# Kernel optimization log

Measured on AMD Instinct MI355X. Metric: run time of the kernel, lower is better.

Reference implementation:

```python
import jax, jax.numpy as jnp
import numpy as np

N = 50000   # nodes
E = 800000  # edges
F = 16      # raw feature width (sliced 4:10 -> 6)
H = 256     # hidden_dim
O = 128     # out_dim
NE = 4      # n_experts
G = 64      # graphs in batch
K = 2       # top_k
XS, XE = 4, 10
SPS = 0.3   # size_prior_strength


def setup_inputs() -> dict:
    key = jax.random.key(0)
    ks = jax.random.split(key, 16)
    rn = lambda k, s: jax.random.normal(k, s, dtype=jnp.float32) * 0.05
    return dict(
        x=jax.random.normal(ks[0], (N, F), dtype=jnp.float32),
        edge_index=jax.random.randint(ks[1], (2, E), 0, N),
        batch=jnp.sort(jax.random.randint(ks[2], (N,), 0, G)),
        enc_W1=rn(ks[3], (6, H)), enc_b1=jnp.zeros(H, jnp.float32),
        enc_W2=rn(ks[4], (H, H)), enc_b2=jnp.zeros(H, jnp.float32),
        r_W1=rn(ks[5], (H + 3, H)), r_b1=jnp.zeros(H, jnp.float32),
        ln_g=jnp.ones(H, jnp.float32), ln_b=jnp.zeros(H, jnp.float32),
        r_W2=rn(ks[6], (H, NE)), r_b2=jnp.zeros(NE, jnp.float32),
        size_centers=jnp.linspace(0.0, 1.0, NE, dtype=jnp.float32),
        W0_rel=rn(ks[7], (NE, H, H)), b0_rel=jnp.zeros((NE, H), jnp.float32), W0_root=rn(ks[8], (NE, H, H)),
        W1_rel=rn(ks[9], (NE, H, H)), b1_rel=jnp.zeros((NE, H), jnp.float32), W1_root=rn(ks[10], (NE, H, H)),
        W2_rel=rn(ks[11], (NE, H, O)), b2_rel=jnp.zeros((NE, O), jnp.float32), W2_root=rn(ks[12], (NE, H, O)),
    )


def _forward(x, edge_index, batch, enc_W1, enc_b1, enc_W2, enc_b2,
             r_W1, r_b1, ln_g, ln_b, r_W2, r_b2, size_centers,
             W0_rel, b0_rel, W0_root, W1_rel, b1_rel, W1_root, W2_rel, b2_rel, W2_root):
    src, dst = edge_index[0], edge_index[1]
    xs = x[:, XS:XE]                                   # [N,6]
    h = jax.nn.relu(xs @ enc_W1 + enc_b1) @ enc_W2 + enc_b2  # [N,H]

    # per-graph size features (bincounts via scatter-add)
    n = jnp.maximum(jnp.zeros(G, jnp.float32).at[batch].add(1.0), 1.0)
    e = jnp.zeros(G, jnp.float32).at[batch[src]].add(1.0)
    density = e / jnp.maximum(n * (n - 1.0), 1.0)
    logn = jnp.log(n)
    logn_norm = (logn - logn.min()) / (logn.max() - logn.min() + 1e-6)
    feats = jnp.stack([n, e, density], -1)             # [G,3]
    feats = (feats - feats.mean(0, keepdims=True)) / (feats.std(0, keepdims=True) + 1e-6)
    sf = feats[batch]                                   # [N,3]
    ln_node = logn_norm[batch]                          # [N]

    # router: Linear -> LayerNorm -> ReLU -> Linear, combined with size prior
    inp = jnp.concatenate([h, sf], -1)                  # [N,H+3]
    t = inp @ r_W1 + r_b1
    t = (t - t.mean(-1, keepdims=True)) * jax.lax.rsqrt(t.var(-1, keepdims=True) + 1e-5) * ln_g + ln_b
    learned = jax.nn.relu(t) @ r_W2 + r_b2              # [N,NE]
    prior = -(ln_node[:, None] - size_centers[None, :]) ** 2
    logits = (1.0 - SPS) * learned + SPS * prior        # temperature = 1.0

    # top-k gate
    probs = jax.nn.softmax(logits, -1)
    top_vals, top_idx = jax.lax.top_k(probs, K)
    top_vals = top_vals / (top_vals.sum(-1, keepdims=True) + 1e-8)
    weights = jnp.zeros_like(probs).at[jnp.arange(N)[:, None], top_idx].set(top_vals)

    # GraphConv experts: out = lin_rel(sum_{j->i} x_j) + lin_root(x_i)
    def aggregate(v):  # [N,C] -> [N,C] scatter-add of src features onto dst
        return jnp.zeros_like(v).at[dst].add(v[src])

    agg_h = aggregate(h)
    hE = jax.nn.relu(jnp.einsum('nh,eho->eno', agg_h, W0_rel) + b0_rel[:, None, :]
                     + jnp.einsum('nh,eho->eno', h, W0_root))            # [NE,N,H]
    aggE = jax.vmap(aggregate)(hE)
    hE = jax.nn.relu(jnp.einsum('enh,eho->eno', aggE, W1_rel) + b1_rel[:, None, :]
                     + jnp.einsum('enh,eho->eno', hE, W1_root))          # [NE,N,H]
    aggE = jax.vmap(aggregate)(hE)
    outE = (jnp.einsum('enh,eho->eno', aggE, W2_rel) + b2_rel[:, None, :]
            + jnp.einsum('enh,eho->eno', hE, W2_root))                   # [NE,N,O]

    return jnp.einsum('eno,ne->no', outE, weights)                       # [N,O]


def reference(x, edge_index, batch, enc_W1, enc_b1, enc_W2, enc_b2,
              r_W1, r_b1, ln_g, ln_b, r_W2, r_b2, size_centers,
              W0_rel, b0_rel, W0_root, W1_rel, b1_rel, W1_root, W2_rel, b2_rel, W2_root):
    return _forward(x, edge_index, batch, enc_W1, enc_b1, enc_W2, enc_b2,
                    r_W1, r_b1, ln_g, ln_b, r_W2, r_b2, size_centers,
                    W0_rel, b0_rel, W0_root, W1_rel, b1_rel, W1_root, W2_rel, b2_rel, W2_root)
```

## Files before the change

### kernel.cpp

```cpp
#include <hip/hip_runtime.h>
#include <hip/hip_bf16.h>

#define H_DIM 256
#define O_DIM 128
#define NEXP 4
#define G_DIM 64

typedef unsigned short ushort_t;
typedef unsigned int uint_t;
typedef __attribute__((ext_vector_type(8))) short short8;
typedef __attribute__((ext_vector_type(4))) float floatx4;

__device__ __forceinline__ float bf2f(ushort_t u) {
    union { uint_t i; float f; } c; c.i = ((uint_t)u) << 16; return c.f;
}
__device__ __forceinline__ ushort_t f2bf(float f) {
    union { float f; uint_t i; } c; c.f = f;
    uint_t x = c.i;
    uint_t r = (x + 0x7fffu + ((x >> 16) & 1u)) >> 16;
    return (ushort_t)r;
}

__device__ __forceinline__ void load16_lds(const void* g, void* l) {
    __builtin_amdgcn_global_load_lds(
        (const __attribute__((address_space(1))) unsigned int*)g,
        (__attribute__((address_space(3))) unsigned int*)l, 16, 0, 0);
}

__global__ void zero_i_kernel(int* __restrict__ p, long n) {
    long i = (long)blockIdx.x * blockDim.x + threadIdx.x;
    if (i < n) p[i] = 0;
}

__global__ void wsplit2_kernel(const float* __restrict__ Wa, const float* __restrict__ Wb,
                               ushort_t* __restrict__ Wh) {
    int z = blockIdx.y;
    int i = blockIdx.x * 256 + threadIdx.x;
    if (i >= 131072) return;
    int nn = i >> 9, kk = i & 511;
    float v = (kk < 256) ? Wa[(long)z * 65536 + kk * 256 + nn]
                         : Wb[(long)z * 65536 + (kk - 256) * 256 + nn];
    Wh[(long)z * 131072 + i] = f2bf(v);
}

__global__ void wsplitcat_kernel(const float* __restrict__ Wa, const float* __restrict__ Wb,
                                 ushort_t* __restrict__ Wh) {
    int z = blockIdx.y;
    int i = blockIdx.x * 256 + threadIdx.x;
    if (i >= 65536) return;
    int nn = i >> 8, kk = i & 255;
    float v = (nn < 128) ? Wa[(long)z * 32768 + kk * 128 + nn]
                         : Wb[(long)z * 32768 + kk * 128 + (nn - 128)];
    Wh[(long)z * 65536 + i] = f2bf(v);
}

__global__ void encoder1_kernel(const float* __restrict__ x, const float* __restrict__ W1,
                                const float* __restrict__ b1, float* __restrict__ u,
                                int N, int F) {
    int n = blockIdx.x;
    int j = threadIdx.x;
    float acc = b1[j];
    #pragma unroll
    for (int c = 0; c < 6; ++c)
        acc += x[(long)n * F + 4 + c] * W1[c * H_DIM + j];
    u[(long)n * H_DIM + j] = fmaxf(acc, 0.f);
}

__global__ __launch_bounds__(256)
void gemm256_kernel(const float* __restrict__ A, const float* __restrict__ W,
                    const float* __restrict__ bias, float* __restrict__ C,
                    ushort_t* __restrict__ Cbf, int M, int Nc) {
    const int K = 256;
    __shared__ float As[16][68];
    __shared__ float Ws[16][68];
    int tid = threadIdx.x;
    int tx = tid & 15, ty = tid >> 4;
    int row0 = blockIdx.x * 64;
    int col0 = blockIdx.y * 64;
    float acc[4][4] = {};
    int lrow = tid >> 2, kq = tid & 3;
    int wk = tid >> 4, wc = (tid & 15) * 4;
    for (int k0 = 0; k0 < K; k0 += 16) {
        float4 av = make_float4(0.f, 0.f, 0.f, 0.f);
        int arow = row0 + lrow;
        if (arow < M) av = *(const float4*)(A + (long)arow * K + k0 + kq * 4);
        As[kq * 4 + 0][lrow] = av.x;
        As[kq * 4 + 1][lrow] = av.y;
        As[kq * 4 + 2][lrow] = av.z;
        As[kq * 4 + 3][lrow] = av.w;
        float4 wv = *(const float4*)(W + (long)(k0 + wk) * Nc + col0 + wc);
        *(float4*)&Ws[wk][wc] = wv;
        __syncthreads();
        #pragma unroll
        for (int kk = 0; kk < 16; ++kk) {
            float a[4], b[4];
            #pragma unroll
            for (int i = 0; i < 4; ++i) a[i] = As[kk][ty * 4 + i];
            #pragma unroll
            for (int j = 0; j < 4; ++j) b[j] = Ws[kk][tx * 4 + j];
            #pragma unroll
            for (int i = 0; i < 4; ++i)
                #pragma unroll
                for (int j = 0; j < 4; ++j) acc[i][j] += a[i] * b[j];
        }
        __syncthreads();
    }
    #pragma unroll
    for (int i = 0; i < 4; ++i) {
        int r = row0 + ty * 4 + i;
        if (r >= M) break;
        #pragma unroll
        for (int j = 0; j < 4; ++j) {
            int c = col0 + tx * 4 + j;
            float v = acc[i][j];
            if (bias) v += bias[c];
            C[(long)r * Nc + c] = v;
            if (Cbf) Cbf[(long)r * Nc + c] = f2bf(v);
        }
    }
}

template<int NH>
__global__ __launch_bounds__(256)
void gemm_bf_kernel(const ushort_t* __restrict__ A1, long sA1z, int rsA1,
                    const ushort_t* __restrict__ A2, long sA2z, int rsA2,
                    const ushort_t* __restrict__ B, long sBz,
                    const float* __restrict__ bias, int sBiasz,
                    ushort_t* __restrict__ Cbf, long sCz, int rsC,
                    int M, int Kb, int relu) {
    __shared__ alignas(16) ushort_t Asl[2][128 * 32];
    __shared__ alignas(16) ushort_t Bsl[2][128 * 32];

    const int tid = threadIdx.x, wave = tid >> 6, lane = tid & 63;
    const int z = blockIdx.z;
    const int row0 = blockIdx.x * 128, col0 = blockIdx.y * 128;
    const int wr = (wave >> 1) * 64, wcx = (wave & 1) * 64;
    floatx4 acc[4][4] = {};

    A1 += (long)z * sA1z;
    A2 += (long)z * sA2z;
    B += (long)z * sBz;
    if (bias) bias += (long)z * sBiasz;
    Cbf += (long)z * sCz;

    const int bsr = lane >> 2;
    const int bgc = ((lane & 3) - (bsr >> 1)) & 3;
    long aoff1[2], aoff2[2];
    #pragma unroll
    for (int q = 0; q < 2; ++q) {
        int ar = row0 + wave * 32 + q * 16 + bsr;
        ar = ar < M ? ar : M - 1;
        aoff1[q] = (long)ar * rsA1 + bgc * 8;
        aoff2[q] = (long)ar * rsA2 + bgc * 8;
    }
    const long brow = (long)(col0 + wave * 32 + bsr) * Kb + bgc * 8;
    const ushort_t* Bg0 = B + brow;
    const ushort_t* Bg1 = B + brow + (long)16 * Kb;
    const int la0 = (wave * 32) * 32;
    const int la1 = (wave * 32 + 16) * 32;

    const int fm = lane & 15, fq = lane >> 4;
    const int NK = NH * 8;

    load16_lds(A1 + aoff1[0], &Asl[0][la0]);
    load16_lds(A1 + aoff1[1], &Asl[0][la1]);
    load16_lds(Bg0, &Bsl[0][la0]);
    load16_lds(Bg1, &Bsl[0][la1]);
    __syncthreads();

    for (int k = 0; k < NK; ++k) {
        const int buf = k & 1;
        short8 a[4], b[4];
        #pragma unroll
        for (int j = 0; j < 4; ++j) {
            int row = wcx + j * 16 + fm;
            int slot = (fq + ((row >> 1) & 3)) & 3;
            b[j] = *(const short8*)&Bsl[buf][row * 32 + slot * 8];
        }
        #pragma unroll
        for (int i = 0; i < 4; ++i) {
            int row = wr + i * 16 + fm;
            int slot = (fq + ((row >> 1) & 3)) & 3;
            a[i] = *(const short8*)&Asl[buf][row * 32 + slot * 8];
        }
        if (k + 1 < NK) {
            const int kn = k + 1, bn = kn & 1;
            const ushort_t* Ab = (kn >> 3) ? A2 : A1;
            const long* ao = (kn >> 3) ? aoff2 : aoff1;
            const int k0 = (kn & 7) * 32;
            const int kk = kn * 32;
            load16_lds(Ab + ao[0] + k0, &Asl[bn][la0]);
            load16_lds(Ab + ao[1] + k0, &Asl[bn][la1]);
            load16_lds(Bg0 + kk, &Bsl[bn][la0]);
            load16_lds(Bg1 + kk, &Bsl[bn][la1]);
        }
        #pragma unroll
        for (int i = 0; i < 4; ++i)
            #pragma unroll
            for (int j = 0; j < 4; ++j)
                acc[i][j] = __builtin_amdgcn_mfma_f32_16x16x32_bf16(a[i], b[j], acc[i][j], 0, 0, 0);
        if (k + 1 < NK) __syncthreads();
    }

    #pragma unroll
    for (int i = 0; i < 4; ++i) {
        #pragma unroll
        for (int j = 0; j < 4; ++j) {
            int col = col0 + wcx + j * 16 + fm;
            int rowb = row0 + wr + i * 16 + fq * 4;
            #pragma unroll
            for (int r = 0; r < 4; ++r) {
                int row = rowb + r;
                if (row < M) {
                    float v = acc[i][j][r];
                    if (bias) v += bias[col];
                    if (relu) v = fmaxf(v, 0.f);
                    Cbf[(long)row * rsC + col] = f2bf(v);
                }
            }
        }
    }
}

__global__ void hist_nodes_kernel(const int* __restrict__ batch, int n, int* __restrict__ gn) {
    __shared__ int bins[G_DIM];
    int t = threadIdx.x;
    if (t < G_DIM) bins[t] = 0;
    __syncthreads();
    for (long i = (long)blockIdx.x * blockDim.x + t; i < n; i += (long)gridDim.x * blockDim.x)
        atomicAdd(&bins[batch[i]], 1);
    __syncthreads();
    if (t < G_DIM) atomicAdd(&gn[t], bins[t]);
}

__global__ void hist_edges_kernel(const int* __restrict__ ei, const int* __restrict__ batch,
                                  int E, int* __restrict__ ge) {
    __shared__ int bins[G_DIM];
    int t = threadIdx.x;
    if (t < G_DIM) bins[t] = 0;
    __syncthreads();
    for (long i = (long)blockIdx.x * blockDim.x + t; i < E; i += (long)gridDim.x * blockDim.x)
        atomicAdd(&bins[batch[ei[i]]], 1);
    __syncthreads();
    if (t < G_DIM) atomicAdd(&ge[t], bins[t]);
}

__global__ void graph_stats_kernel(const int* __restrict__ gn, const int* __restrict__ ge,
                                   float* __restrict__ feats_norm, float* __restrict__ logn_norm) {
    int g = threadIdx.x;
    float nv = fmaxf((float)gn[g], 1.0f);
    float ev = (float)ge[g];
    float density = ev / fmaxf(nv * (nv - 1.0f), 1.0f);
    float logn = logf(nv);
    float mn = logn, mx = logn;
    for (int o = 32; o; o >>= 1) {
        mn = fminf(mn, __shfl_xor(mn, o));
        mx = fmaxf(mx, __shfl_xor(mx, o));
    }
    logn_norm[g] = (logn - mn) / (mx - mn + 1e-6f);
    float f[3] = {nv, ev, density};
    #pragma unroll
    for (int c = 0; c < 3; ++c) {
        float s = f[c];
        for (int o = 32; o; o >>= 1) s += __shfl_xor(s, o);
        float mean = s / 64.f;
        float d = f[c] - mean;
        float v = d * d;
        for (int o = 32; o; o >>= 1) v += __shfl_xor(v, o);
        float stdv = sqrtf(v / 64.f);
        feats_norm[g * 3 + c] = d / (stdv + 1e-6f);
    }
}

__global__ __launch_bounds__(256)
void router_epi_kernel(const float* __restrict__ t, const int* __restrict__ batch,
                       const float* __restrict__ feats_norm, const float* __restrict__ logn_norm,
                       const float* __restrict__ rW1, const float* __restrict__ rb1,
                       const float* __restrict__ lng, const float* __restrict__ lnb,
                       const float* __restrict__ rW2, const float* __restrict__ rb2,
                       const float* __restrict__ centers, float* __restrict__ w, int N) {
    int wave = threadIdx.x >> 6, lane = threadIdx.x & 63;
    int n = blockIdx.x * 4 + wave;
    if (n >= N) return;
    int g = batch[n];
    float sf0 = feats_norm[g * 3 + 0], sf1 = feats_norm[g * 3 + 1], sf2 = feats_norm[g * 3 + 2];
    float ln = logn_norm[g];
    float tv[4];
    #pragma unroll
    for (int q = 0; q < 4; ++q) {
        int j = lane + 64 * q;
        tv[q] = t[(long)n * H_DIM + j] + rb1[j]
              + sf0 * rW1[256 * H_DIM + j] + sf1 * rW1[257 * H_DIM + j] + sf2 * rW1[258 * H_DIM + j];
    }
    float s = tv[0] + tv[1] + tv[2] + tv[3];
    for (int o = 32; o; o >>= 1) s += __shfl_xor(s, o);
    float mean = s / 256.f;
    float vs = 0.f;
    #pragma unroll
    for (int q = 0; q < 4; ++q) { float d = tv[q] - mean; vs += d * d; }
    for (int o = 32; o; o >>= 1) vs += __shfl_xor(vs, o);
    float rstd = rsqrtf(vs / 256.f + 1e-5f);
    float le[NEXP] = {0.f, 0.f, 0.f, 0.f};
    #pragma unroll
    for (int q = 0; q < 4; ++q) {
        int j = lane + 64 * q;
        float y = (tv[q] - mean) * rstd * lng[j] + lnb[j];
        y = fmaxf(y, 0.f);
        #pragma unroll
        for (int e = 0; e < NEXP; ++e) le[e] += y * rW2[j * NEXP + e];
    }
    #pragma unroll
    for (int e = 0; e < NEXP; ++e)
        for (int o = 32; o; o >>= 1) le[e] += __shfl_xor(le[e], o);
    if (lane == 0) {
        float p[NEXP];
        float m = -1e30f;
        #pragma unroll
        for (int e = 0; e < NEXP; ++e) {
            float d = ln - centers[e];
            float lv = 0.7f * (le[e] + rb2[e]) + 0.3f * (-(d * d));
            p[e] = lv;
            m = fmaxf(m, lv);
        }
        float ssum = 0.f;
        #pragma unroll
        for (int e = 0; e < NEXP; ++e) { p[e] = expf(p[e] - m); ssum += p[e]; }
        #pragma unroll
        for (int e = 0; e < NEXP; ++e) p[e] /= ssum;
        int i1 = 0;
        for (int e = 1; e < NEXP; ++e) if (p[e] > p[i1]) i1 = e;
        int i2 = -1;
        for (int e = 0; e < NEXP; ++e) { if (e == i1) continue; if (i2 < 0 || p[e] > p[i2]) i2 = e; }
        float denom = p[i1] + p[i2] + 1e-8f;
        float out4[NEXP] = {0.f, 0.f, 0.f, 0.f};
        out4[i1] = p[i1] / denom;
        out4[i2] = p[i2] / denom;
        #pragma unroll
        for (int e = 0; e < NEXP; ++e) w[(long)n * NEXP + e] = out4[e];
    }
}

__global__ void count_dst_kernel(const int* __restrict__ ei, int E, int* __restrict__ cnt) {
    int i = blockIdx.x * blockDim.x + threadIdx.x;
    if (i < E) atomicAdd(&cnt[ei[E + i]], 1);
}

__global__ __launch_bounds__(1024)
void scan_kernel(const int* __restrict__ cnt, int* __restrict__ row_ptr, int n) {
    __shared__ int buf[1024];
    __shared__ int carry_s;
    int tid = threadIdx.x;
    if (tid == 0) carry_s = 0;
    __syncthreads();
    for (int base = 0; base < n; base += 1024) {
        int v = (base + tid < n) ? cnt[base + tid] : 0;
        buf[tid] = v;
        __syncthreads();
        for (int off = 1; off < 1024; off <<= 1) {
            int tv = (tid >= off) ? buf[tid - off] : 0;
            __syncthreads();
            buf[tid] += tv;
            __syncthreads();
        }
        int carry = carry_s;
        if (base + tid < n) row_ptr[base + tid] = carry + buf[tid] - v;
        __syncthreads();
        if (tid == 1023) carry_s = carry + buf[1023];
        __syncthreads();
    }
    if (tid == 0) row_ptr[n] = carry_s;
}

__global__ void fill_csr_kernel(const int* __restrict__ ei, int E, const int* __restrict__ row_ptr,
                                int* __restrict__ fillc, int* __restrict__ srcs) {
    int i = blockIdx.x * blockDim.x + threadIdx.x;
    if (i < E) {
        int d = ei[E + i];
        int pos = row_ptr[d] + atomicAdd(&fillc[d], 1);
        srcs[pos] = ei[i];
    }
}

__global__ __launch_bounds__(256)
void agg_b2b_kernel(const ushort_t* __restrict__ feat, ushort_t* __restrict__ outp,
                    const int* __restrict__ rp, const int* __restrict__ srcs, int N) {
    int wave = threadIdx.x >> 6, lane = threadIdx.x & 63;
    int n = blockIdx.x * 4 + wave;
    if (n >= N) return;
    float a0 = 0.f, a1 = 0.f, a2 = 0.f, a3 = 0.f;
    int p0 = rp[n], p1 = rp[n + 1];
    const ushort_t* base = feat + lane * 4;
    int p = p0;
    for (; p + 3 < p1; p += 4) {
        uint2 v0 = *(const uint2*)(base + (long)srcs[p] * H_DIM);
        uint2 v1 = *(const uint2*)(base + (long)srcs[p + 1] * H_DIM);
        uint2 v2 = *(const uint2*)(base + (long)srcs[p + 2] * H_DIM);
        uint2 v3 = *(const uint2*)(base + (long)srcs[p + 3] * H_DIM);
        a0 += bf2f((ushort_t)(v0.x & 0xffff)) + bf2f((ushort_t)(v1.x & 0xffff))
            + bf2f((ushort_t)(v2.x & 0xffff)) + bf2f((ushort_t)(v3.x & 0xffff));
        a1 += bf2f((ushort_t)(v0.x >> 16)) + bf2f((ushort_t)(v1.x >> 16))
            + bf2f((ushort_t)(v2.x >> 16)) + bf2f((ushort_t)(v3.x >> 16));
        a2 += bf2f((ushort_t)(v0.y & 0xffff)) + bf2f((ushort_t)(v1.y & 0xffff))
            + bf2f((ushort_t)(v2.y & 0xffff)) + bf2f((ushort_t)(v3.y & 0xffff));
        a3 += bf2f((ushort_t)(v0.y >> 16)) + bf2f((ushort_t)(v1.y >> 16))
            + bf2f((ushort_t)(v2.y >> 16)) + bf2f((ushort_t)(v3.y >> 16));
    }
    for (; p < p1; ++p) {
        uint2 v = *(const uint2*)(base + (long)srcs[p] * H_DIM);
        a0 += bf2f((ushort_t)(v.x & 0xffff));
        a1 += bf2f((ushort_t)(v.x >> 16));
        a2 += bf2f((ushort_t)(v.y & 0xffff));
        a3 += bf2f((ushort_t)(v.y >> 16));
    }
    uint2 o;
    o.x = (uint_t)f2bf(a0) | ((uint_t)f2bf(a1) << 16);
    o.y = (uint_t)f2bf(a2) | ((uint_t)f2bf(a3) << 16);
    *(uint2*)(outp + (long)n * H_DIM + lane * 4) = o;
}

__global__ void aggI_kernel(const ushort_t* __restrict__ feat, ushort_t* __restrict__ outp,
                            const int* __restrict__ rp, const int* __restrict__ srcs,
                            int N, int W) {
    int n = blockIdx.x;
    int t = threadIdx.x;
    float a[8] = {0.f, 0.f, 0.f, 0.f, 0.f, 0.f, 0.f, 0.f};
    int p0 = rp[n], p1 = rp[n + 1];
    const ushort_t* base = feat + t * 8;
    int p = p0;
    for (; p + 3 < p1; p += 4) {
        uint4 v0 = *(const uint4*)(base + (long)srcs[p] * W);
        uint4 v1 = *(const uint4*)(base + (long)srcs[p + 1] * W);
        uint4 v2 = *(const uint4*)(base + (long)srcs[p + 2] * W);
        uint4 v3 = *(const uint4*)(base + (long)srcs[p + 3] * W);
        uint_t w0[4] = {v0.x, v0.y, v0.z, v0.w};
        uint_t w1[4] = {v1.x, v1.y, v1.z, v1.w};
        uint_t w2[4] = {v2.x, v2.y, v2.z, v2.w};
        uint_t w3[4] = {v3.x, v3.y, v3.z, v3.w};
        #pragma unroll
        for (int q = 0; q < 4; ++q) {
            a[2 * q]     += bf2f((ushort_t)(w0[q] & 0xffff)) + bf2f((ushort_t)(w1[q] & 0xffff))
                          + bf2f((ushort_t)(w2[q] & 0xffff)) + bf2f((ushort_t)(w3[q] & 0xffff));
            a[2 * q + 1] += bf2f((ushort_t)(w0[q] >> 16)) + bf2f((ushort_t)(w1[q] >> 16))
                          + bf2f((ushort_t)(w2[q] >> 16)) + bf2f((ushort_t)(w3[q] >> 16));
        }
    }
    for (; p < p1; ++p) {
        uint4 v = *(const uint4*)(base + (long)srcs[p] * W);
        uint_t w[4] = {v.x, v.y, v.z, v.w};
        #pragma unroll
        for (int q = 0; q < 4; ++q) {
            a[2 * q]     += bf2f((ushort_t)(w[q] & 0xffff));
            a[2 * q + 1] += bf2f((ushort_t)(w[q] >> 16));
        }
    }
    uint4 o;
    o.x = (uint_t)f2bf(a[0]) | ((uint_t)f2bf(a[1]) << 16);
    o.y = (uint_t)f2bf(a[2]) | ((uint_t)f2bf(a[3]) << 16);
    o.z = (uint_t)f2bf(a[4]) | ((uint_t)f2bf(a[5]) << 16);
    o.w = (uint_t)f2bf(a[6]) | ((uint_t)f2bf(a[7]) << 16);
    *(uint4*)(outp + (long)n * W + t * 8) = o;
}

__global__ __launch_bounds__(256)
void final_mixE_kernel(const ushort_t* __restrict__ PR, const float* __restrict__ b2,
                       const float* __restrict__ wts, int e0, int EB,
                       const int* __restrict__ rp, const int* __restrict__ srcs,
                       float* __restrict__ out, int N, int init) {
    int wave = threadIdx.x >> 6, lane = threadIdx.x & 63;
    int n = blockIdx.x * 4 + wave;
    if (n >= N) return;
    const int W = EB * 256;
    int c0 = lane * 2;
    long obase = (long)n * O_DIM + c0;
    float o0 = init ? 0.f : out[obase];
    float o1 = init ? 0.f : out[obase + 1];
    int zs[2]; float wv[2]; int na = 0;
    for (int z = 0; z < EB; ++z) {
        float w = wts[(long)n * NEXP + e0 + z];
        if (w != 0.f && na < 2) { zs[na] = z; wv[na] = w; ++na; }
    }
    if (na) {
        const ushort_t* P0 = PR + zs[0] * 256 + c0;
        const ushort_t* P1 = PR + zs[na - 1] * 256 + c0;
        float a00 = 0.f, a01 = 0.f, a10 = 0.f, a11 = 0.f;
        int p0 = rp[n], p1 = rp[n + 1];
        if (na == 2) {
            int p = p0;
            for (; p + 1 < p1; p += 2) {
                long s0 = (long)srcs[p] * W;
                long s1 = (long)srcs[p + 1] * W;
                uint_t v00 = *(const uint_t*)(P0 + s0);
                uint_t v10 = *(const uint_t*)(P1 + s0);
                uint_t v01 = *(const uint_t*)(P0 + s1);
                uint_t v11 = *(const uint_t*)(P1 + s1);
                a00 += bf2f((ushort_t)(v00 & 0xffff)) + bf2f((ushort_t)(v01 & 0xffff));
                a01 += bf2f((ushort_t)(v00 >> 16))    + bf2f((ushort_t)(v01 >> 16));
                a10 += bf2f((ushort_t)(v10 & 0xffff)) + bf2f((ushort_t)(v11 & 0xffff));
                a11 += bf2f((ushort_t)(v10 >> 16))    + bf2f((ushort_t)(v11 >> 16));
            }
            if (p < p1) {
                long s = (long)srcs[p] * W;
                uint_t v0 = *(const uint_t*)(P0 + s);
                uint_t v1 = *(const uint_t*)(P1 + s);
                a00 += bf2f((ushort_t)(v0 & 0xffff)); a01 += bf2f((ushort_t)(v0 >> 16));
                a10 += bf2f((ushort_t)(v1 & 0xffff)); a11 += bf2f((ushort_t)(v1 >> 16));
            }
        } else {
            int p = p0;
            for (; p + 3 < p1; p += 4) {
                uint_t v0 = *(const uint_t*)(P0 + (long)srcs[p] * W);
                uint_t v1 = *(const uint_t*)(P0 + (long)srcs[p + 1] * W);
                uint_t v2 = *(const uint_t*)(P0 + (long)srcs[p + 2] * W);
                uint_t v3 = *(const uint_t*)(P0 + (long)srcs[p + 3] * W);
                a00 += bf2f((ushort_t)(v0 & 0xffff)) + bf2f((ushort_t)(v1 & 0xffff))
                     + bf2f((ushort_t)(v2 & 0xffff)) + bf2f((ushort_t)(v3 & 0xffff));
                a01 += bf2f((ushort_t)(v0 >> 16)) + bf2f((ushort_t)(v1 >> 16))
                     + bf2f((ushort_t)(v2 >> 16)) + bf2f((ushort_t)(v3 >> 16));
            }
            for (; p < p1; ++p) {
                uint_t v = *(const uint_t*)(P0 + (long)srcs[p] * W);
                a00 += bf2f((ushort_t)(v & 0xffff)); a01 += bf2f((ushort_t)(v >> 16));
            }
        }
        {
            int e = e0 + zs[0];
            uint_t rv = *(const uint_t*)(PR + (long)n * W + zs[0] * 256 + 128 + c0);
            o0 += wv[0] * (a00 + bf2f((ushort_t)(rv & 0xffff)) + b2[e * O_DIM + c0]);
            o1 += wv[0] * (a01 + bf2f((ushort_t)(rv >> 16))    + b2[e * O_DIM + c0 + 1]);
        }
        if (na == 2) {
            int e = e0 + zs[1];
            uint_t rv = *(const uint_t*)(PR + (long)n * W + zs[1] * 256 + 128 + c0);
            o0 += wv[1] * (a10 + bf2f((ushort_t)(rv & 0xffff)) + b2[e * O_DIM + c0]);
            o1 += wv[1] * (a11 + bf2f((ushort_t)(rv >> 16))    + b2[e * O_DIM + c0 + 1]);
        }
    }
    out[obase] = o0;
    out[obase + 1] = o1;
}

extern "C" void kernel_launch(void* const* d_in, const int* in_sizes, int n_in,
                              void* d_out, int out_size, void* d_ws, size_t ws_size,
                              hipStream_t stream) {
    const float* x       = (const float*)d_in[0];
    const int*   ei      = (const int*)  d_in[1];
    const int*   batch   = (const int*)  d_in[2];
    const float* enc_W1  = (const float*)d_in[3];
    const float* enc_b1  = (const float*)d_in[4];
    const float* enc_W2  = (const float*)d_in[5];
    const float* enc_b2  = (const float*)d_in[6];
    const float* r_W1    = (const float*)d_in[7];
    const float* r_b1    = (const float*)d_in[8];
    const float* ln_g    = (const float*)d_in[9];
    const float* ln_b    = (const float*)d_in[10];
    const float* r_W2    = (const float*)d_in[11];
    const float* r_b2    = (const float*)d_in[12];
    const float* centers = (const float*)d_in[13];
    const float* W0_rel  = (const float*)d_in[14];
    const float* b0_rel  = (const float*)d_in[15];
    const float* W0_root = (const float*)d_in[16];
    const float* W1_rel  = (const float*)d_in[17];
    const float* b1_rel  = (const float*)d_in[18];
    const float* W1_root = (const float*)d_in[19];
    const float* W2_rel  = (const float*)d_in[20];
    const float* b2_rel  = (const float*)d_in[21];
    const float* W2_root = (const float*)d_in[22];

    const int N = in_sizes[2];
    const int E = in_sizes[1] / 2;
    const int F = in_sizes[0] / N;

    char* ws = (char*)d_ws;
    size_t off = 0;
    auto alloc = [&](size_t bytes) -> void* {
        void* p = ws + off;
        off += (bytes + 255) & ~(size_t)255;
        return p;
    };
    int* cnt      = (int*)alloc((size_t)N * 4);
    int* fillc    = (int*)alloc((size_t)N * 4);
    int* gn       = (int*)alloc((size_t)G_DIM * 4);
    int* ge       = (int*)alloc((size_t)G_DIM * 4);
    size_t zero_bytes = off;
    int* row_ptr  = (int*)alloc((size_t)(N + 1) * 4);
    int* srcs     = (int*)alloc((size_t)E * 4);
    float* feats_norm = (float*)alloc((size_t)G_DIM * 3 * 4);
    float* logn_norm  = (float*)alloc((size_t)G_DIM * 4);
    float* wts    = (float*)alloc((size_t)N * NEXP * 4);
    ushort_t* wf0  = (ushort_t*)alloc((size_t)NEXP * 131072 * 2);
    ushort_t* wf1  = (ushort_t*)alloc((size_t)NEXP * 131072 * 2);
    ushort_t* wfin = (ushort_t*)alloc((size_t)NEXP * 65536 * 2);
    const long sE = (long)N * H_DIM;
    ushort_t* h_bf    = (ushort_t*)alloc((size_t)sE * 2);
    ushort_t* aggh_bf = (ushort_t*)alloc((size_t)sE * 2);
    size_t fixed_end = off;
    size_t slab4 = ((size_t)4 * sE * 2 + 255) & ~(size_t)255;
    int EB = (ws_size >= fixed_end + 3 * slab4 + (1u << 20)) ? 4 : 2;
    size_t slab = ((size_t)EB * sE * 2 + 255) & ~(size_t)255;
    ushort_t* S1 = (ushort_t*)alloc(slab);
    ushort_t* S2 = (ushort_t*)alloc(slab);
    ushort_t* S3 = (ushort_t*)alloc(slab);
    (void)out_size; (void)n_in;

    float* u    = (float*)S1;
    float* h    = (float*)S2;
    float* tf32 = (float*)S3;
    ushort_t* hE0  = S1;
    ushort_t* aggE = S2;
    ushort_t* hE1  = S3;
    ushort_t* PR   = S2;
    float* out = (float*)d_out;

    const int W  = EB * 256;
    dim3 blk256(256);
    dim3 gR((N + 63) / 64, H_DIM / 64, 1);
    dim3 gM((N + 127) / 128, 2, EB);
    dim3 gAgg((N + 3) / 4);

    {
        long nz = (long)(zero_bytes / 4);
        zero_i_kernel<<<dim3((nz + 255) / 256), blk256, 0, stream>>>((int*)ws, nz);
    }
    wsplit2_kernel<<<dim3(512, NEXP), blk256, 0, stream>>>(W0_rel, W0_root, wf0);
    wsplit2_kernel<<<dim3(512, NEXP), blk256, 0, stream>>>(W1_rel, W1_root, wf1);
    wsplitcat_kernel<<<dim3(256, NEXP), blk256, 0, stream>>>(W2_rel, W2_root, wfin);
    encoder1_kernel<<<dim3(N), blk256, 0, stream>>>(x, enc_W1, enc_b1, u, N, F);
    gemm256_kernel<<<gR, blk256, 0, stream>>>(u, enc_W2, enc_b2, h, h_bf, N, H_DIM);
    hist_nodes_kernel<<<dim3(256), blk256, 0, stream>>>(batch, N, gn);
    hist_edges_kernel<<<dim3(512), blk256, 0, stream>>>(ei, batch, E, ge);
    graph_stats_kernel<<<dim3(1), dim3(64), 0, stream>>>(gn, ge, feats_norm, logn_norm);
    gemm256_kernel<<<gR, blk256, 0, stream>>>(h, r_W1, nullptr, tf32, nullptr, N, H_DIM);
    router_epi_kernel<<<dim3((N + 3) / 4), blk256, 0, stream>>>(
        tf32, batch, feats_norm, logn_norm, r_W1, r_b1, ln_g, ln_b, r_W2, r_b2, centers, wts, N);
    count_dst_kernel<<<dim3((E + 255) / 256), blk256, 0, stream>>>(ei, E, cnt);
    scan_kernel<<<dim3(1), dim3(1024), 0, stream>>>(cnt, row_ptr, N);
    fill_csr_kernel<<<dim3((E + 255) / 256), blk256, 0, stream>>>(ei, E, row_ptr, fillc, srcs);
    agg_b2b_kernel<<<gAgg, blk256, 0, stream>>>(h_bf, aggh_bf, row_ptr, srcs, N);

    for (int b = 0; b < NEXP / EB; ++b) {
        const int e0 = b * EB;
        gemm_bf_kernel<2><<<gM, blk256, 0, stream>>>(
            aggh_bf, 0, 256, h_bf, 0, 256,
            wf0 + (long)e0 * 131072, 131072,
            b0_rel + e0 * H_DIM, H_DIM, hE0, 256, W, N, 512, 1);
        aggI_kernel<<<dim3(N), dim3(W / 8), 0, stream>>>(hE0, aggE, row_ptr, srcs, N, W);
        gemm_bf_kernel<2><<<gM, blk256, 0, stream>>>(
            aggE, 256, W, hE0, 256, W,
            wf1 + (long)e0 * 131072, 131072,
            b1_rel + e0 * H_DIM, H_DIM, hE1, 256, W, N, 512, 1);
        gemm_bf_kernel<1><<<gM, blk256, 0, stream>>>(
            hE1, 256, W, nullptr, 0, 256,
            wfin + (long)e0 * 65536, 65536,
            nullptr, 0, PR, 256, W, N, 256, 0);
        final_mixE_kernel<<<gAgg, blk256, 0, stream>>>(
            PR, b2_rel, wts, e0, EB, row_ptr, srcs, out, N, b == 0 ? 1 : 0);
    }
}
```

Before: 1.294 ms.

## Shrink expert GEMM row tile to 64 and compact workspace so 4-expert batching fits

The bf16 MFMA expert GEMM now uses 64x128 output tiles instead of 128x128, with half the A-tile shared memory and half the accumulators per wave. This doubles the grid and lowers register and LDS pressure, which should help occupancy and latency hiding, at the cost of reloading B tiles more often. The workspace layout also changes: when the 4-expert path is taken, h_bf, aggh_bf and the fp32 router temp are placed inside the third slab, so the larger batching needs less memory. PR is moved to alias S1, which relies on the lifetimes of the aliased buffers not overlapping.

```diff
diff --git a/kernel.cpp b/kernel.cpp
--- a/kernel.cpp
+++ b/kernel.cpp
@@ -128,14 +128,14 @@
                     const float* __restrict__ bias, int sBiasz,
                     ushort_t* __restrict__ Cbf, long sCz, int rsC,
                     int M, int Kb, int relu) {
-    __shared__ alignas(16) ushort_t Asl[2][128 * 32];
+    __shared__ alignas(16) ushort_t Asl[2][64 * 32];
     __shared__ alignas(16) ushort_t Bsl[2][128 * 32];
 
     const int tid = threadIdx.x, wave = tid >> 6, lane = tid & 63;
     const int z = blockIdx.z;
-    const int row0 = blockIdx.x * 128, col0 = blockIdx.y * 128;
-    const int wr = (wave >> 1) * 64, wcx = (wave & 1) * 64;
-    floatx4 acc[4][4] = {};
+    const int row0 = blockIdx.x * 64, col0 = blockIdx.y * 128;
+    const int wr = (wave >> 1) * 32, wcx = (wave & 1) * 64;
+    floatx4 acc[2][4] = {};
 
     A1 += (long)z * sA1z;
     A2 += (long)z * sA2z;
@@ -145,32 +145,31 @@
 
     const int bsr = lane >> 2;
     const int bgc = ((lane & 3) - (bsr >> 1)) & 3;
-    long aoff1[2], aoff2[2];
-    #pragma unroll
-    for (int q = 0; q < 2; ++q) {
-        int ar = row0 + wave * 32 + q * 16 + bsr;
+    long aoff1, aoff2;
+    {
+        int ar = row0 + wave * 16 + bsr;
         ar = ar < M ? ar : M - 1;
-        aoff1[q] = (long)ar * rsA1 + bgc * 8;
-        aoff2[q] = (long)ar * rsA2 + bgc * 8;
+        aoff1 = (long)ar * rsA1 + bgc * 8;
+        aoff2 = (long)ar * rsA2 + bgc * 8;
     }
     const long brow = (long)(col0 + wave * 32 + bsr) * Kb + bgc * 8;
     const ushort_t* Bg0 = B + brow;
     const ushort_t* Bg1 = B + brow + (long)16 * Kb;
-    const int la0 = (wave * 32) * 32;
-    const int la1 = (wave * 32 + 16) * 32;
+    const int laA  = (wave * 16) * 32;
+    const int laB0 = (wave * 32) * 32;
+    const int laB1 = (wave * 32 + 16) * 32;
 
     const int fm = lane & 15, fq = lane >> 4;
     const int NK = NH * 8;
 
-    load16_lds(A1 + aoff1[0], &Asl[0][la0]);
-    load16_lds(A1 + aoff1[1], &Asl[0][la1]);
-    load16_lds(Bg0, &Bsl[0][la0]);
-    load16_lds(Bg1, &Bsl[0][la1]);
+    load16_lds(A1 + aoff1, &Asl[0][laA]);
+    load16_lds(Bg0, &Bsl[0][laB0]);
+    load16_lds(Bg1, &Bsl[0][laB1]);
     __syncthreads();
 
     for (int k = 0; k < NK; ++k) {
         const int buf = k & 1;
-        short8 a[4], b[4];
+        short8 a[2], b[4];
         #pragma unroll
         for (int j = 0; j < 4; ++j) {
             int row = wcx + j * 16 + fm;
@@ -178,7 +177,7 @@
             b[j] = *(const short8*)&Bsl[buf][row * 32 + slot * 8];
         }
         #pragma unroll
-        for (int i = 0; i < 4; ++i) {
+        for (int i = 0; i < 2; ++i) {
             int row = wr + i * 16 + fm;
             int slot = (fq + ((row >> 1) & 3)) & 3;
             a[i] = *(const short8*)&Asl[buf][row * 32 + slot * 8];
@@ -186,16 +185,15 @@
         if (k + 1 < NK) {
             const int kn = k + 1, bn = kn & 1;
             const ushort_t* Ab = (kn >> 3) ? A2 : A1;
-            const long* ao = (kn >> 3) ? aoff2 : aoff1;
+            const long ao = (kn >> 3) ? aoff2 : aoff1;
             const int k0 = (kn & 7) * 32;
             const int kk = kn * 32;
-            load16_lds(Ab + ao[0] + k0, &Asl[bn][la0]);
-            load16_lds(Ab + ao[1] + k0, &Asl[bn][la1]);
-            load16_lds(Bg0 + kk, &Bsl[bn][la0]);
-            load16_lds(Bg1 + kk, &Bsl[bn][la1]);
-        }
-        #pragma unroll
-        for (int i = 0; i < 4; ++i)
+            load16_lds(Ab + ao + k0, &Asl[bn][laA]);
+            load16_lds(Bg0 + kk, &Bsl[bn][laB0]);
+            load16_lds(Bg1 + kk, &Bsl[bn][laB1]);
+        }
+        #pragma unroll
+        for (int i = 0; i < 2; ++i)
             #pragma unroll
             for (int j = 0; j < 4; ++j)
                 acc[i][j] = __builtin_amdgcn_mfma_f32_16x16x32_bf16(a[i], b[j], acc[i][j], 0, 0, 0);
@@ -203,7 +201,7 @@
     }
 
     #pragma unroll
-    for (int i = 0; i < 4; ++i) {
+    for (int i = 0; i < 2; ++i) {
         #pragma unroll
         for (int j = 0; j < 4; ++j) {
             int col = col0 + wcx + j * 16 + fm;
@@ -590,31 +588,45 @@
     ushort_t* wf0  = (ushort_t*)alloc((size_t)NEXP * 131072 * 2);
     ushort_t* wf1  = (ushort_t*)alloc((size_t)NEXP * 131072 * 2);
     ushort_t* wfin = (ushort_t*)alloc((size_t)NEXP * 65536 * 2);
+
     const long sE = (long)N * H_DIM;
-    ushort_t* h_bf    = (ushort_t*)alloc((size_t)sE * 2);
-    ushort_t* aggh_bf = (ushort_t*)alloc((size_t)sE * 2);
     size_t fixed_end = off;
     size_t slab4 = ((size_t)4 * sE * 2 + 255) & ~(size_t)255;
-    int EB = (ws_size >= fixed_end + 3 * slab4 + (1u << 20)) ? 4 : 2;
-    size_t slab = ((size_t)EB * sE * 2 + 255) & ~(size_t)255;
-    ushort_t* S1 = (ushort_t*)alloc(slab);
-    ushort_t* S2 = (ushort_t*)alloc(slab);
-    ushort_t* S3 = (ushort_t*)alloc(slab);
+    size_t slab2 = ((size_t)2 * sE * 2 + 255) & ~(size_t)255;
+    size_t need4 = fixed_end + 3 * slab4 + (1u << 20);
+
+    int EB;
+    ushort_t *S1, *S2, *S3, *h_bf, *aggh_bf;
+    float *u, *h, *tf32;
+    if (ws_size >= need4) {
+        EB = 4;
+        S1 = (ushort_t*)alloc(slab4);
+        S2 = (ushort_t*)alloc(slab4);
+        S3 = (ushort_t*)alloc(slab4);
+        u = (float*)S1; h = (float*)S2;
+        h_bf = S3; aggh_bf = S3 + sE;
+        tf32 = (float*)(S3 + 2 * sE);
+    } else {
+        EB = 2;
+        h_bf    = (ushort_t*)alloc((size_t)sE * 2);
+        aggh_bf = (ushort_t*)alloc((size_t)sE * 2);
+        S1 = (ushort_t*)alloc(slab2);
+        S2 = (ushort_t*)alloc(slab2);
+        S3 = (ushort_t*)alloc(slab2);
+        u = (float*)S1; h = (float*)S2; tf32 = (float*)S3;
+    }
     (void)out_size; (void)n_in;
 
-    float* u    = (float*)S1;
-    float* h    = (float*)S2;
-    float* tf32 = (float*)S3;
     ushort_t* hE0  = S1;
     ushort_t* aggE = S2;
     ushort_t* hE1  = S3;
-    ushort_t* PR   = S2;
+    ushort_t* PR   = S1;
     float* out = (float*)d_out;
 
     const int W  = EB * 256;
     dim3 blk256(256);
     dim3 gR((N + 63) / 64, H_DIM / 64, 1);
-    dim3 gM((N + 127) / 128, 2, EB);
+    dim3 gM((N + 63) / 64, 2, EB);
     dim3 gAgg((N + 3) / 4);
 
     {
```

Measured after the change: 1.263 ms. 1.02x faster.
